# Kernel tuning notes

Measured on AMD Instinct MI355X. Metric: run time of the kernel, lower is better.

Reference implementation:

```python
import jax, jax.numpy as jnp
import numpy as np

DIM = 1024
NUM_HEADS = 16
HEAD_DIM = DIM // NUM_HEADS
SCALE = HEAD_DIM ** -0.5


def setup_inputs() -> dict:
    key = jax.random.key(0)
    ks = jax.random.split(key, 5)
    B, N = 2, 2048
    x = jax.random.normal(ks[0], (B, N, DIM), dtype=jnp.float32)
    # nn.Linear weights: stored as [out, in]; we keep that convention.
    w_qkv = jax.random.normal(ks[1], (3 * DIM, DIM), dtype=jnp.float32) * (DIM ** -0.5)
    b_qkv = jax.random.normal(ks[2], (3 * DIM,), dtype=jnp.float32) * 0.02
    w_proj = jax.random.normal(ks[3], (DIM, DIM), dtype=jnp.float32) * (DIM ** -0.5)
    b_proj = jax.random.normal(ks[4], (DIM,), dtype=jnp.float32) * 0.02
    return {"x": x, "w_qkv": w_qkv, "b_qkv": b_qkv, "w_proj": w_proj, "b_proj": b_proj}


def reference(x, w_qkv, b_qkv, w_proj, b_proj):
    B, N, C = x.shape
    H, D = NUM_HEADS, HEAD_DIM
    qkv = x @ w_qkv.T + b_qkv                      # [B, N, 3C]
    qkv = qkv.reshape(B, N, 3, H, D)
    q = qkv[:, :, 0].transpose(0, 2, 1, 3)         # [B, H, N, D]
    k = qkv[:, :, 1].transpose(0, 2, 1, 3)
    v = qkv[:, :, 2].transpose(0, 2, 1, 3)
    attn = jnp.einsum("bhnd,bhmd->bhnm", q, k) * SCALE  # [B, H, N, N]
    attn = jax.nn.softmax(attn, axis=-1)
    out = jnp.einsum("bhnm,bhmd->bhnd", attn, v)   # [B, H, N, D]
    out = out.transpose(0, 2, 1, 3).reshape(B, N, C)
    return out @ w_proj.T + b_proj
```

## Files before the change

### kernel.cpp

```cpp
#include <hip/hip_runtime.h>
#include <math.h>

#define DIMC   1024
#define NHEADS 16
#define HDIM   64
#define BATCH  2
#define SEQ    2048

#define MTOT   (BATCH * SEQ)
#define QKVN   (3 * DIMC)
#define QKVSZ  ((size_t)BATCH * NHEADS * SEQ * HDIM)
#define HEADEL ((size_t)SEQ * HDIM)

#define QSCALE 0.18033688011112042f

typedef __attribute__((ext_vector_type(8))) short bf16x8;
typedef __attribute__((ext_vector_type(4))) short bf16x4;
typedef __attribute__((ext_vector_type(4))) float f32x4;

static __device__ inline short f2bf(float f) {
    union { float f; unsigned u; } v; v.f = f;
    unsigned r = v.u + 0x7fffu + ((v.u >> 16) & 1u);
    return (short)(r >> 16);
}
static __device__ inline short f2bf_fast(float f) {
    union { float f; unsigned u; } v; v.f = f;
    return (short)((v.u + 0x8000u) >> 16);
}

#if __has_builtin(__builtin_amdgcn_exp2f)
#define EXP2F(x) __builtin_amdgcn_exp2f(x)
#else
#define EXP2F(x) exp2f(x)
#endif

#define NXB  (MTOT * DIMC / 2048)
#define NWQB (QKVN * DIMC / 2048)
#define NWPB (DIMC * DIMC / 2048)

__global__ __launch_bounds__(256) void cast_all(
    const float* __restrict__ x,  const float* __restrict__ wq,
    const float* __restrict__ wp, short* __restrict__ xb,
    short* __restrict__ wqb, short* __restrict__ wpb)
{
    const float* in; short* out; int base;
    int bid = blockIdx.x;
    if (bid < NXB)              { in = x;  out = xb;  base = bid; }
    else if (bid < NXB + NWQB)  { in = wq; out = wqb; base = bid - NXB; }
    else                        { in = wp; out = wpb; base = bid - NXB - NWQB; }
    int i = (base * 256 + threadIdx.x) * 8;
    float4 a = *(const float4*)&in[i];
    float4 b = *(const float4*)&in[i + 4];
    bf16x8 o;
    o[0] = f2bf(a.x); o[1] = f2bf(a.y); o[2] = f2bf(a.z); o[3] = f2bf(a.w);
    o[4] = f2bf(b.x); o[5] = f2bf(b.y); o[6] = f2bf(b.z); o[7] = f2bf(b.w);
    *(bf16x8*)&out[i] = o;
}

__device__ __forceinline__ void gload16(const void* g, void* l) {
    __builtin_amdgcn_global_load_lds(
        (const __attribute__((address_space(1))) unsigned*)g,
        (__attribute__((address_space(3))) unsigned*)l, 16, 0, 0);
}

__device__ __forceinline__ void mfma_kloop64(
    const short* __restrict__ A, const short* __restrict__ B,
    int m0, int j0, short* Asm, short* Bsm, int tid, f32x4 acc[4][4])
{
    const int lane = tid & 63;
    const int w    = tid >> 6;
    const int quad = lane >> 4;
    const int lid  = lane & 15;
    const int wm = (w >> 1) * 64, wn = (w & 1) * 64;

    const int srow = lane >> 2;
    const int skc  = (lane & 3) * 8;

    for (int k0 = 0; k0 < 1024; k0 += 64) {
        __syncthreads();
#pragma unroll
        for (int u = 0; u < 4; ++u) {
            const int combo = w * 4 + u;
            const int hh = combo >> 3, rb = combo & 7;
            const int row = rb * 16 + srow;
            gload16(&A[(size_t)(m0 + row) * 1024 + k0 + hh * 32 + skc],
                    &Asm[hh * 4096 + row * 32 + skc]);
            gload16(&B[(size_t)(j0 + row) * 1024 + k0 + hh * 32 + skc],
                    &Bsm[hh * 4096 + row * 32 + skc]);
        }
        __syncthreads();

#pragma unroll
        for (int hh = 0; hh < 2; ++hh) {
            bf16x8 af[4], bfr[4];
#pragma unroll
            for (int i = 0; i < 4; ++i)
                af[i] = *(const bf16x8*)&Asm[hh * 4096 + (wm + i * 16 + lid) * 32 + quad * 8];
#pragma unroll
            for (int j = 0; j < 4; ++j)
                bfr[j] = *(const bf16x8*)&Bsm[hh * 4096 + (wn + j * 16 + lid) * 32 + quad * 8];
#pragma unroll
            for (int i = 0; i < 4; ++i)
#pragma unroll
                for (int j = 0; j < 4; ++j)
                    acc[i][j] = __builtin_amdgcn_mfma_f32_16x16x32_bf16(
                        af[i], bfr[j], acc[i][j], 0, 0, 0);
        }
    }
}

__global__ __launch_bounds__(256) void qkv_mfma(
    const short* __restrict__ xb,
    const short* __restrict__ wb,
    const float* __restrict__ bias,
    short* __restrict__ qkvb)
{
    __shared__ __attribute__((aligned(16))) short Asm[2 * 128 * 32];
    __shared__ __attribute__((aligned(16))) short Bsm[2 * 128 * 32];

    const int tid = threadIdx.x;
    const int m0 = blockIdx.y * 128;
    const int j0 = blockIdx.x * 128;

    f32x4 acc[4][4];
#pragma unroll
    for (int i = 0; i < 4; ++i)
#pragma unroll
        for (int j = 0; j < 4; ++j) acc[i][j] = (f32x4){0.f, 0.f, 0.f, 0.f};

    mfma_kloop64(xb, wb, m0, j0, Asm, Bsm, tid, acc);

    const int lane = tid & 63;
    const int w    = tid >> 6;
    const int quad = lane >> 4;
    const int lid  = lane & 15;
    const int wm = (w >> 1) * 64, wn = (w & 1) * 64;
    const int s = j0 >> 10;

    if (s == 0) {
#pragma unroll
        for (int jb = 0; jb < 4; ++jb) {
            const int jj = j0 + wn + jb * 16 + lid;
            const int hh = (jj & 1023) >> 6;
            const int dd = jj & 63;
            const float bv = bias[jj];
#pragma unroll
            for (int i = 0; i < 4; ++i)
#pragma unroll
                for (int r = 0; r < 4; ++r) {
                    const int mrow = m0 + wm + i * 16 + quad * 4 + r;
                    const int b_ = mrow >> 11, nn = mrow & 2047;
                    qkvb[((size_t)(b_ * NHEADS + hh) * SEQ + nn) * HDIM + dd] =
                        f2bf((acc[i][jb][r] + bv) * QSCALE);
                }
        }
    } else if (s == 1) {
#pragma unroll
        for (int jb = 0; jb < 4; ++jb) {
            const int jj = j0 + wn + jb * 16 + lid;
            const int hh = (jj & 1023) >> 6;
            const int dd = jj & 63;
            const int c2 = dd >> 5;
            const int qd = (dd >> 3) & 3;
            const int jo = dd & 7;
            const float bv = bias[jj];
#pragma unroll
            for (int i = 0; i < 4; ++i) {
                const int mrow0 = m0 + wm + i * 16;
                const int b_ = mrow0 >> 11;
                const int n0 = mrow0 & 2047;
                const int t32 = n0 >> 5;
                const int i16 = (n0 >> 4) & 1;
                const int c = quad & 1;
                const int lidb = (i16 * 2 + (quad >> 1)) * 4;
                size_t base = QKVSZ + (size_t)(b_ * NHEADS + hh) * HEADEL +
                              (size_t)(t32 * 4 + c2 * 2 + c) * 512 +
                              (qd * 16 + lidb) * 8 + jo;
#pragma unroll
                for (int r = 0; r < 4; ++r)
                    qkvb[base + r * 8] = f2bf(acc[i][jb][r] + bv);
            }
        }
    } else {
#pragma unroll
        for (int jb = 0; jb < 4; ++jb) {
            const int jj = j0 + wn + jb * 16 + lid;
            const int hh = (jj & 1023) >> 6;
            const int dd = jj & 63;
            const int fb = dd >> 4;
            const int dl = dd & 15;
            const float bv = bias[jj];
#pragma unroll
            for (int i = 0; i < 4; ++i) {
                const int mrow0 = m0 + wm + i * 16 + quad * 4;
                const int b_ = mrow0 >> 11, n0 = mrow0 & 2047;
                const int t32 = n0 >> 5;
                const int i16 = (n0 >> 4) & 1;
                const int quadpp = i16 * 2 + (quad >> 1);
                bf16x4 o;
#pragma unroll
                for (int r = 0; r < 4; ++r) o[r] = f2bf(acc[i][jb][r] + bv);
                *(bf16x4*)&qkvb[2 * QKVSZ + (size_t)(b_ * NHEADS + hh) * HEADEL +
                                (size_t)(t32 * 4 + fb) * 512 +
                                (quadpp * 16 + dl) * 8 + (quad & 1) * 4] = o;
            }
        }
    }
}

__global__ __launch_bounds__(256, 2) void attn_mfma(
    const short* __restrict__ qkvb,
    short* __restrict__ aob)
{
    __shared__ float Osm[2][4][4][4][64];
    __shared__ float Lsm[3][64];

    const int tid  = threadIdx.x;
    const int sp   = tid >> 6;
    const int lane = tid & 63;
    const int quad = lane >> 4;
    const int lid  = lane & 15;

    const int qbase = blockIdx.x * 64;
    const int h  = blockIdx.y;
    const int b  = blockIdx.z;

    const short* Qh = qkvb + (size_t)(b * NHEADS + h) * HEADEL;
    const short* Kf = Qh + QKVSZ;
    const short* Vf = qkvb + 2 * QKVSZ + (size_t)(b * NHEADS + h) * HEADEL;

    bf16x8 bQ[4][2];
#pragma unroll
    for (int g = 0; g < 4; ++g)
#pragma unroll
        for (int c = 0; c < 2; ++c)
            bQ[g][c] = *(const bf16x8*)&Qh[(size_t)(qbase + g * 16 + lid) * HDIM +
                                           c * 32 + quad * 8];

    f32x4 O[4][4];
    f32x4 L[4];
#pragma unroll
    for (int g = 0; g < 4; ++g) {
        L[g] = (f32x4){0.f, 0.f, 0.f, 0.f};
#pragma unroll
        for (int fb = 0; fb < 4; ++fb) O[g][fb] = (f32x4){0.f, 0.f, 0.f, 0.f};
    }
    const bf16x8 ones8 = {(short)0x3F80, (short)0x3F80, (short)0x3F80, (short)0x3F80,
                          (short)0x3F80, (short)0x3F80, (short)0x3F80, (short)0x3F80};

#pragma unroll 2
    for (int cc = 0; cc < SEQ / 128; ++cc) {
        const int t = sp * (SEQ / 128) + cc;
        bf16x8 aK[2][2];
#pragma unroll
        for (int c = 0; c < 2; ++c)
#pragma unroll
            for (int c2 = 0; c2 < 2; ++c2)
                aK[c][c2] = *(const bf16x8*)&Kf[(size_t)(t * 4 + c2 * 2 + c) * 512 +
                                                lane * 8];
        bf16x8 aV[4];
#pragma unroll
        for (int fb = 0; fb < 4; ++fb)
            aV[fb] = *(const bf16x8*)&Vf[(size_t)(t * 4 + fb) * 512 + lane * 8];

#pragma unroll
        for (int g = 0; g < 4; ++g) {
            f32x4 s0 = (f32x4){0.f, 0.f, 0.f, 0.f};
            f32x4 s1 = (f32x4){0.f, 0.f, 0.f, 0.f};
            s0 = __builtin_amdgcn_mfma_f32_16x16x32_bf16(aK[0][0], bQ[g][0], s0, 0, 0, 0);
            s1 = __builtin_amdgcn_mfma_f32_16x16x32_bf16(aK[1][0], bQ[g][0], s1, 0, 0, 0);
            s0 = __builtin_amdgcn_mfma_f32_16x16x32_bf16(aK[0][1], bQ[g][1], s0, 0, 0, 0);
            s1 = __builtin_amdgcn_mfma_f32_16x16x32_bf16(aK[1][1], bQ[g][1], s1, 0, 0, 0);
            bf16x8 P;
#pragma unroll
            for (int r = 0; r < 4; ++r) {
                P[r]     = f2bf_fast(EXP2F(s0[r]));
                P[4 + r] = f2bf_fast(EXP2F(s1[r]));
            }
            L[g] = __builtin_amdgcn_mfma_f32_16x16x32_bf16(ones8, P, L[g], 0, 0, 0);
#pragma unroll
            for (int fb = 0; fb < 4; ++fb)
                O[g][fb] = __builtin_amdgcn_mfma_f32_16x16x32_bf16(
                    aV[fb], P, O[g][fb], 0, 0, 0);
        }
    }

    if (sp != 0 && quad == 0)
#pragma unroll
        for (int g = 0; g < 4; ++g) Lsm[sp - 1][g * 16 + lid] = L[g][0];

    if (sp == 1 || sp == 3) {
        const int buf = sp >> 1;
#pragma unroll
        for (int g = 0; g < 4; ++g)
#pragma unroll
            for (int fb = 0; fb < 4; ++fb)
#pragma unroll
                for (int r = 0; r < 4; ++r)
                    Osm[buf][g][fb][r][lane] = O[g][fb][r];
    }
    __syncthreads();
    if (sp == 0 || sp == 2) {
        const int buf = sp >> 1;
#pragma unroll
        for (int g = 0; g < 4; ++g)
#pragma unroll
            for (int fb = 0; fb < 4; ++fb)
#pragma unroll
                for (int r = 0; r < 4; ++r)
                    O[g][fb][r] += Osm[buf][g][fb][r][lane];
    }
    __syncthreads();
    if (sp == 2) {
#pragma unroll
        for (int g = 0; g < 4; ++g)
#pragma unroll
            for (int fb = 0; fb < 4; ++fb)
#pragma unroll
                for (int r = 0; r < 4; ++r)
                    Osm[0][g][fb][r][lane] = O[g][fb][r];
    }
    __syncthreads();
    if (sp == 0) {
#pragma unroll
        for (int g = 0; g < 4; ++g) {
            const float lt = L[g][0] + Lsm[0][g * 16 + lid] +
                             Lsm[1][g * 16 + lid] + Lsm[2][g * 16 + lid];
            const float inv = 1.f / lt;
            const int n = qbase + g * 16 + lid;
            size_t base = ((size_t)(b * SEQ + n)) * DIMC + h * HDIM;
#pragma unroll
            for (int fb = 0; fb < 4; ++fb) {
                bf16x4 o;
#pragma unroll
                for (int r = 0; r < 4; ++r)
                    o[r] = f2bf((O[g][fb][r] + Osm[0][g][fb][r][lane]) * inv);
                *(bf16x4*)&aob[base + fb * 16 + quad * 4] = o;
            }
        }
    }
}

__global__ __launch_bounds__(256, 2) void proj_mfma(
    const short* __restrict__ ab,
    const short* __restrict__ wb,
    const float* __restrict__ bias,
    float* __restrict__ out)
{
    __shared__ __attribute__((aligned(16))) short Asm[2 * 64 * 32];
    __shared__ __attribute__((aligned(16))) short Bsm[2 * 128 * 32];

    const int tid = threadIdx.x;
    const int m0 = blockIdx.y * 64;
    const int j0 = blockIdx.x * 128;

    const int lane = tid & 63;
    const int w    = tid >> 6;
    const int quad = lane >> 4;
    const int lid  = lane & 15;
    const int wm = (w >> 1) * 32, wn = (w & 1) * 64;

    const int srow = lane >> 2;
    const int skc  = (lane & 3) * 8;

    f32x4 acc[2][4];
#pragma unroll
    for (int i = 0; i < 2; ++i)
#pragma unroll
        for (int j = 0; j < 4; ++j) acc[i][j] = (f32x4){0.f, 0.f, 0.f, 0.f};

    for (int k0 = 0; k0 < 1024; k0 += 64) {
        __syncthreads();
#pragma unroll
        for (int u = 0; u < 2; ++u) {
            const int combo = w * 2 + u;
            const int hh = combo >> 2, rb = combo & 3;
            const int row = rb * 16 + srow;
            gload16(&ab[(size_t)(m0 + row) * 1024 + k0 + hh * 32 + skc],
                    &Asm[hh * 2048 + row * 32 + skc]);
        }
#pragma unroll
        for (int u = 0; u < 4; ++u) {
            const int combo = w * 4 + u;
            const int hh = combo >> 3, rb = combo & 7;
            const int row = rb * 16 + srow;
            gload16(&wb[(size_t)(j0 + row) * 1024 + k0 + hh * 32 + skc],
                    &Bsm[hh * 4096 + row * 32 + skc]);
        }
        __syncthreads();

#pragma unroll
        for (int hh = 0; hh < 2; ++hh) {
            bf16x8 af[2], bfr[4];
#pragma unroll
            for (int i = 0; i < 2; ++i)
                af[i] = *(const bf16x8*)&Asm[hh * 2048 + (wm + i * 16 + lid) * 32 + quad * 8];
#pragma unroll
            for (int j = 0; j < 4; ++j)
                bfr[j] = *(const bf16x8*)&Bsm[hh * 4096 + (wn + j * 16 + lid) * 32 + quad * 8];
#pragma unroll
            for (int i = 0; i < 2; ++i)
#pragma unroll
                for (int j = 0; j < 4; ++j)
                    acc[i][j] = __builtin_amdgcn_mfma_f32_16x16x32_bf16(
                        af[i], bfr[j], acc[i][j], 0, 0, 0);
        }
    }

#pragma unroll
    for (int jb = 0; jb < 4; ++jb) {
        const int jj = j0 + wn + jb * 16 + lid;
        const float bv = bias[jj];
#pragma unroll
        for (int i = 0; i < 2; ++i)
#pragma unroll
            for (int r = 0; r < 4; ++r) {
                const int mrow = m0 + wm + i * 16 + quad * 4 + r;
                out[(size_t)mrow * DIMC + jj] = acc[i][jb][r] + bv;
            }
    }
}

extern "C" void kernel_launch(void* const* d_in, const int* in_sizes, int n_in,
                              void* d_out, int out_size, void* d_ws, size_t ws_size,
                              hipStream_t stream) {
    const float* x      = (const float*)d_in[0];
    const float* w_qkv  = (const float*)d_in[1];
    const float* b_qkv  = (const float*)d_in[2];
    const float* w_proj = (const float*)d_in[3];
    const float* b_proj = (const float*)d_in[4];
    float* out = (float*)d_out;

    short* qkvb   = (short*)d_ws;
    short* xb     = qkvb + 3 * QKVSZ;
    short* wqkvb  = xb + (size_t)MTOT * DIMC;
    short* wprojb = wqkvb + (size_t)QKVN * DIMC;
    short* aob    = wprojb + (size_t)DIMC * DIMC;

    cast_all<<<NXB + NWQB + NWPB, 256, 0, stream>>>(x, w_qkv, w_proj,
                                                    xb, wqkvb, wprojb);

    dim3 g1(QKVN / 128, MTOT / 128);
    qkv_mfma<<<g1, 256, 0, stream>>>(xb, wqkvb, b_qkv, qkvb);

    dim3 g2(SEQ / 64, NHEADS, BATCH);
    attn_mfma<<<g2, 256, 0, stream>>>(qkvb, aob);

    dim3 g3(DIMC / 128, MTOT / 64);
    proj_mfma<<<g3, 256, 0, stream>>>(aob, wprojb, b_proj, out);
}
```

Measured before the change: 186.6 us.

## Rewrite QKV GEMM with 256x256 tiles, double-buffered LDS and swizzle

The QKV projection GEMM moves from 128x128 tiles on 256 threads to 256x256 tiles on 512 threads. It uses 128 KB of dynamic LDS, double-buffered with the next k-slice prefetched through global_load_lds, and an XOR-swizzled LDS layout to avoid bank conflicts. Compute is split into four barrier-separated phases with raised wave priority around the MFMAs, and the 192 blocks are remapped for locality. The intent is to hide global-load latency and improve data reuse per tile. In exchange, each block uses far more LDS and registers, fewer blocks run at once, and the single wave of 192 blocks may leave some CUs idle.

```diff
diff --git a/kernel.cpp b/kernel.cpp
--- a/kernel.cpp
+++ b/kernel.cpp
@@ -63,78 +63,130 @@
         (__attribute__((address_space(3))) unsigned*)l, 16, 0, 0);
 }
 
-__device__ __forceinline__ void mfma_kloop64(
-    const short* __restrict__ A, const short* __restrict__ B,
-    int m0, int j0, short* Asm, short* Bsm, int tid, f32x4 acc[4][4])
+#define BAR() do { __builtin_amdgcn_s_barrier(); \
+                   __builtin_amdgcn_sched_barrier(0); } while (0)
+#define VWAIT8() asm volatile("s_waitcnt vmcnt(8)" ::: "memory")
+#define VWAIT0() asm volatile("s_waitcnt vmcnt(0)" ::: "memory")
+
+__device__ __forceinline__ void stage_panel(const short* __restrict__ src,
+                                            int row0, int k0,
+                                            short* dst, int tid)
 {
-    const int lane = tid & 63;
-    const int w    = tid >> 6;
-    const int quad = lane >> 4;
-    const int lid  = lane & 15;
-    const int wm = (w >> 1) * 64, wn = (w & 1) * 64;
-
-    const int srow = lane >> 2;
-    const int skc  = (lane & 3) * 8;
-
-    for (int k0 = 0; k0 < 1024; k0 += 64) {
-        __syncthreads();
-#pragma unroll
-        for (int u = 0; u < 4; ++u) {
-            const int combo = w * 4 + u;
-            const int hh = combo >> 3, rb = combo & 7;
-            const int row = rb * 16 + srow;
-            gload16(&A[(size_t)(m0 + row) * 1024 + k0 + hh * 32 + skc],
-                    &Asm[hh * 4096 + row * 32 + skc]);
-            gload16(&B[(size_t)(j0 + row) * 1024 + k0 + hh * 32 + skc],
-                    &Bsm[hh * 4096 + row * 32 + skc]);
-        }
-        __syncthreads();
-
-#pragma unroll
-        for (int hh = 0; hh < 2; ++hh) {
-            bf16x8 af[4], bfr[4];
-#pragma unroll
-            for (int i = 0; i < 4; ++i)
-                af[i] = *(const bf16x8*)&Asm[hh * 4096 + (wm + i * 16 + lid) * 32 + quad * 8];
-#pragma unroll
-            for (int j = 0; j < 4; ++j)
-                bfr[j] = *(const bf16x8*)&Bsm[hh * 4096 + (wn + j * 16 + lid) * 32 + quad * 8];
-#pragma unroll
-            for (int i = 0; i < 4; ++i)
-#pragma unroll
-                for (int j = 0; j < 4; ++j)
-                    acc[i][j] = __builtin_amdgcn_mfma_f32_16x16x32_bf16(
-                        af[i], bfr[j], acc[i][j], 0, 0, 0);
-        }
-    }
-}
-
-__global__ __launch_bounds__(256) void qkv_mfma(
+#pragma unroll
+    for (int u = 0; u < 2; ++u) {
+        const int gidx = u * 512 + tid;
+        const int rl   = gidx >> 3;
+        const int cc   = gidx & 7;
+        gload16(&src[(size_t)(row0 + rl) * 1024 + k0 + ((cc ^ (rl & 7)) << 3)],
+                &dst[(size_t)gidx << 3]);
+    }
+}
+
+template<int MH, int NH>
+__device__ __forceinline__ void phase_compute(
+    const short* As, const short* Bs,
+    int wm, int wn, int lid, int quad, f32x4 (&acc)[8][4])
+{
+    bf16x8 af[4][2], bfr[2][2];
+#pragma unroll
+    for (int i2 = 0; i2 < 4; ++i2) {
+        const int r = wm + (MH * 4 + i2) * 16 + lid;
+#pragma unroll
+        for (int kk = 0; kk < 2; ++kk)
+            af[i2][kk] = *(const bf16x8*)
+                &As[r * 64 + (((kk * 4 + quad) ^ (r & 7)) << 3)];
+    }
+#pragma unroll
+    for (int j2 = 0; j2 < 2; ++j2) {
+        const int rb = wn + (NH * 2 + j2) * 16 + lid;
+#pragma unroll
+        for (int kk = 0; kk < 2; ++kk)
+            bfr[j2][kk] = *(const bf16x8*)
+                &Bs[rb * 64 + (((kk * 4 + quad) ^ (rb & 7)) << 3)];
+    }
+    __builtin_amdgcn_s_setprio(1);
+#pragma unroll
+    for (int i2 = 0; i2 < 4; ++i2)
+#pragma unroll
+        for (int j2 = 0; j2 < 2; ++j2)
+#pragma unroll
+            for (int kk = 0; kk < 2; ++kk)
+                acc[MH * 4 + i2][NH * 2 + j2] =
+                    __builtin_amdgcn_mfma_f32_16x16x32_bf16(
+                        af[i2][kk], bfr[j2][kk],
+                        acc[MH * 4 + i2][NH * 2 + j2], 0, 0, 0);
+    __builtin_amdgcn_s_setprio(0);
+}
+
+__global__ __launch_bounds__(512, 2) void qkv_mfma(
     const short* __restrict__ xb,
     const short* __restrict__ wb,
     const float* __restrict__ bias,
     short* __restrict__ qkvb)
 {
-    __shared__ __attribute__((aligned(16))) short Asm[2 * 128 * 32];
-    __shared__ __attribute__((aligned(16))) short Bsm[2 * 128 * 32];
+    extern __shared__ short lds[];
 
     const int tid = threadIdx.x;
-    const int m0 = blockIdx.y * 128;
-    const int j0 = blockIdx.x * 128;
-
-    f32x4 acc[4][4];
-#pragma unroll
-    for (int i = 0; i < 4; ++i)
-#pragma unroll
-        for (int j = 0; j < 4; ++j) acc[i][j] = (f32x4){0.f, 0.f, 0.f, 0.f};
-
-    mfma_kloop64(xb, wb, m0, j0, Asm, Bsm, tid, acc);
+    const int T  = (blockIdx.x & 7) * 24 + (blockIdx.x >> 3);
+    const int m0 = (T / 12) * 256;
+    const int j0 = (T % 12) * 256;
 
     const int lane = tid & 63;
     const int w    = tid >> 6;
     const int quad = lane >> 4;
     const int lid  = lane & 15;
-    const int wm = (w >> 1) * 64, wn = (w & 1) * 64;
+    const int wm = (w >> 2) * 128;
+    const int wn = (w & 3) * 64;
+
+    f32x4 acc[8][4];
+#pragma unroll
+    for (int i = 0; i < 8; ++i)
+#pragma unroll
+        for (int j = 0; j < 4; ++j) acc[i][j] = (f32x4){0.f, 0.f, 0.f, 0.f};
+
+    stage_panel(xb, m0,       0, lds,                 tid);
+    stage_panel(xb, m0 + 128, 0, lds + 8192,          tid);
+    stage_panel(wb, j0,       0, lds + 32768,         tid);
+    stage_panel(wb, j0 + 128, 0, lds + 32768 + 8192,  tid);
+
+#pragma unroll 2
+    for (int kt = 0; kt < 15; ++kt) {
+        const int cb = (kt & 1) << 14;
+        const int nb = (~kt & 1) << 14;
+        const int k1 = (kt + 1) << 6;
+        const short* Ac = lds + cb;
+        const short* Bc = lds + 32768 + cb;
+        short* An = lds + nb;
+        short* Bn = lds + 32768 + nb;
+
+        stage_panel(xb, m0,       k1, An,        tid);
+        stage_panel(xb, m0 + 128, k1, An + 8192, tid);
+        stage_panel(wb, j0,       k1, Bn,        tid);
+        stage_panel(wb, j0 + 128, k1, Bn + 8192, tid);
+
+        VWAIT8(); BAR();
+        phase_compute<0, 0>(Ac, Bc, wm, wn, lid, quad, acc);
+        BAR();
+        phase_compute<0, 1>(Ac, Bc, wm, wn, lid, quad, acc);
+        BAR();
+        phase_compute<1, 0>(Ac, Bc, wm, wn, lid, quad, acc);
+        BAR();
+        phase_compute<1, 1>(Ac, Bc, wm, wn, lid, quad, acc);
+        BAR();
+    }
+    {
+        const short* Ac = lds + 16384;
+        const short* Bc = lds + 32768 + 16384;
+        VWAIT0(); BAR();
+        phase_compute<0, 0>(Ac, Bc, wm, wn, lid, quad, acc);
+        BAR();
+        phase_compute<0, 1>(Ac, Bc, wm, wn, lid, quad, acc);
+        BAR();
+        phase_compute<1, 0>(Ac, Bc, wm, wn, lid, quad, acc);
+        BAR();
+        phase_compute<1, 1>(Ac, Bc, wm, wn, lid, quad, acc);
+    }
+
     const int s = j0 >> 10;
 
     if (s == 0) {
@@ -145,7 +197,7 @@
             const int dd = jj & 63;
             const float bv = bias[jj];
 #pragma unroll
-            for (int i = 0; i < 4; ++i)
+            for (int i = 0; i < 8; ++i)
 #pragma unroll
                 for (int r = 0; r < 4; ++r) {
                     const int mrow = m0 + wm + i * 16 + quad * 4 + r;
@@ -165,7 +217,7 @@
             const int jo = dd & 7;
             const float bv = bias[jj];
 #pragma unroll
-            for (int i = 0; i < 4; ++i) {
+            for (int i = 0; i < 8; ++i) {
                 const int mrow0 = m0 + wm + i * 16;
                 const int b_ = mrow0 >> 11;
                 const int n0 = mrow0 & 2047;
@@ -191,7 +243,7 @@
             const int dl = dd & 15;
             const float bv = bias[jj];
 #pragma unroll
-            for (int i = 0; i < 4; ++i) {
+            for (int i = 0; i < 8; ++i) {
                 const int mrow0 = m0 + wm + i * 16 + quad * 4;
                 const int b_ = mrow0 >> 11, n0 = mrow0 & 2047;
                 const int t32 = n0 >> 5;
@@ -437,11 +489,13 @@
     short* wprojb = wqkvb + (size_t)QKVN * DIMC;
     short* aob    = wprojb + (size_t)DIMC * DIMC;
 
+    hipFuncSetAttribute((const void*)qkv_mfma,
+                        hipFuncAttributeMaxDynamicSharedMemorySize, 131072);
+
     cast_all<<<NXB + NWQB + NWPB, 256, 0, stream>>>(x, w_qkv, w_proj,
                                                     xb, wqkvb, wprojb);
 
-    dim3 g1(QKVN / 128, MTOT / 128);
-    qkv_mfma<<<g1, 256, 0, stream>>>(xb, wqkvb, b_qkv, qkvb);
+    qkv_mfma<<<192, 512, 131072, stream>>>(xb, wqkvb, b_qkv, qkvb);
 
     dim3 g2(SEQ / 64, NHEADS, BATCH);
     attn_mfma<<<g2, 256, 0, stream>>>(qkvb, aob);
```

Result: faster. 181.6 us (-2.7%).
